# Kernel optimization log

Hardware: AMD Instinct MI355X
Metric: run time of the kernel (lower is better)

Reference implementation:

```python
import jax, jax.numpy as jnp
import numpy as np

N = 16384      # number of points
DIM = 128      # feature dim
POS_DIM = 3
K = 16         # neighbors (init kwarg k)
SCALE = np.float32(np.sqrt(DIM))


def setup_inputs() -> dict:
    key = jax.random.key(0)
    ks = jax.random.split(key, 16)
    g = lambda i, shape: (jax.random.normal(ks[i], shape, dtype=jnp.float32) * 0.05)
    return {
        "x": jax.random.normal(ks[0], (N, DIM), dtype=jnp.float32),
        "pos": jax.random.uniform(ks[1], (N, POS_DIM), dtype=jnp.float32),
        # weights stored as (in, out); torch Linear applies x @ W.T + b
        "Wq": g(2, (DIM, DIM)),
        "Wk": g(3, (DIM, DIM)),
        "Wv": g(4, (DIM, DIM)),
        "mid_w1": g(5, (DIM, DIM)), "mid_b1": g(6, (DIM,)),
        "mid_w2": g(7, (DIM, DIM)), "mid_b2": g(8, (DIM,)),
        "pe_w1": g(9, (POS_DIM, DIM)), "pe_b1": g(10, (DIM,)),
        "pe_w2": g(11, (DIM, DIM)), "pe_b2": g(12, (DIM,)),
        "fin_w": g(13, (DIM, DIM)), "fin_b": g(14, (DIM,)),
    }


def _knn_indices(pos):
    # squared pairwise distances [N, N]; top-K smallest -> neighbor indices [N, K]
    sq = jnp.sum(pos * pos, axis=-1)
    d2 = sq[:, None] + sq[None, :] - 2.0 * (pos @ pos.T)
    _, ind = jax.lax.top_k(-d2, K)
    return ind


def reference(x, pos, Wq, Wk, Wv, mid_w1, mid_b1, mid_w2, mid_b2,
              pe_w1, pe_b1, pe_w2, pe_b2, fin_w, fin_b):
    ind = _knn_indices(pos)                    # [N, K] int32 (constant wrt grads)
    x_k = x[ind]                               # [N, K, D]
    pos_k = pos[ind]                           # [N, K, 3]
    rel = pos[:, None, :] - pos_k              # [N, K, 3]
    pe = jax.nn.relu(rel @ pe_w1 + pe_b1) @ pe_w2 + pe_b2    # [N, K, D]
    q = x @ Wq                                 # [N, D]
    h = q[:, None, :] - (x_k @ Wk) + pe        # [N, K, D]
    y = jax.nn.relu(h @ mid_w1 + mid_b1) @ mid_w2 + mid_b2   # [N, K, D]
    y = jax.nn.softmax(y / SCALE, axis=-2)     # softmax over neighbors K
    z = x_k @ Wv + pe                          # [N, K, D]
    agg = jnp.sum(y * z, axis=-2)              # [N, D]
    return agg @ fin_w + fin_b + x
```

## Files before the change

kernel.cpp:

```cpp
#include <hip/hip_runtime.h>
#include <hip/hip_bf16.h>

#define N_PTS 16384
#define DIMF  128
#define KNB   16
#define GRES  8
#define NCELL (GRES*GRES*GRES)

typedef __attribute__((ext_vector_type(8))) short bf16x8;
typedef __attribute__((ext_vector_type(4))) short bf16x4;
typedef __attribute__((ext_vector_type(4))) float f32x4;
typedef __attribute__((ext_vector_type(4))) unsigned int u32x4;
typedef __attribute__((ext_vector_type(2))) unsigned int u32x2;

__device__ __forceinline__ unsigned short f2b(float f){
  unsigned int u = __float_as_uint(f);
  u = u + 0x7fffu + ((u >> 16) & 1u);
  return (unsigned short)(u >> 16);
}
__device__ __forceinline__ unsigned cvtpk(float lo, float hi){
  unsigned r;
  asm("v_cvt_pk_bf16_f32 %0, %1, %2" : "=v"(r) : "v"(lo), "v"(hi));
  return r;
}
__device__ __forceinline__ float b2f(unsigned short u){
  return __uint_as_float(((unsigned)u) << 16);
}
__device__ __forceinline__ float b2fs(short s){
  return __uint_as_float(((unsigned)(unsigned short)s) << 16);
}
__device__ __forceinline__ float unsort_f(unsigned s){
  unsigned u = (s & 0x80000000u) ? (s ^ 0x80000000u) : ~s;
  return __uint_as_float(u);
}

__global__ __launch_bounds__(256) void count_kernel(const float* __restrict__ pos, int* __restrict__ cnt){
  int i = blockIdx.x*256 + threadIdx.x;
  float px = pos[i*3+0], py = pos[i*3+1], pz = pos[i*3+2];
  int cx = min(GRES-1, max(0,(int)(px*(float)GRES)));
  int cy = min(GRES-1, max(0,(int)(py*(float)GRES)));
  int cz = min(GRES-1, max(0,(int)(pz*(float)GRES)));
  atomicAdd(&cnt[(cz*GRES+cy)*GRES+cx], 1);
}

__global__ __launch_bounds__(256) void scan_kernel(const int* __restrict__ cnt, int* __restrict__ starts, int* __restrict__ fillp){
  __shared__ int wsum[4];
  int t = threadIdx.x;
  int lane = t & 63, w = t >> 6;
  int a = cnt[2*t], b = cnt[2*t+1];
  int s = a + b;
  int p = s;
  #pragma unroll
  for (int off = 1; off < 64; off <<= 1){
    int v = __shfl_up(p, off, 64);
    if (lane >= off) p += v;
  }
  if (lane == 63) wsum[w] = p;
  __syncthreads();
  int base = 0;
  for (int i = 0; i < w; ++i) base += wsum[i];
  int excl = base + p - s;
  starts[2*t]   = excl;     fillp[2*t]   = excl;
  starts[2*t+1] = excl + a; fillp[2*t+1] = excl + a;
}

__global__ __launch_bounds__(256) void scatter_kernel(const float* __restrict__ pos, int* __restrict__ fillp,
                                                      float4* __restrict__ pos4, int* __restrict__ pidx,
                                                      int* __restrict__ inv){
  int i = blockIdx.x*256 + threadIdx.x;
  float px = pos[i*3+0], py = pos[i*3+1], pz = pos[i*3+2];
  int cx = min(GRES-1, max(0,(int)(px*(float)GRES)));
  int cy = min(GRES-1, max(0,(int)(py*(float)GRES)));
  int cz = min(GRES-1, max(0,(int)(pz*(float)GRES)));
  int c = (cz*GRES+cy)*GRES+cx;
  float sq = __fadd_rn(__fadd_rn(__fmul_rn(px,px), __fmul_rn(py,py)), __fmul_rn(pz,pz));
  int s = atomicAdd(&fillp[c], 1);
  pos4[s] = make_float4(px, py, pz, sq);
  pidx[s] = i;
  inv[i] = s;
}

__global__ __launch_bounds__(256) void knn_query64(const float4* __restrict__ pos4, const int* __restrict__ pidx,
                                                   const int* __restrict__ starts, const int* __restrict__ cnt,
                                                   const int* __restrict__ inv,
                                                   int* __restrict__ ind_slot, char* __restrict__ flags){
  __shared__ unsigned long long cand[4][64];
  int lane = threadIdx.x & 63;
  int wv   = threadIdx.x >> 6;
  int t = blockIdx.x*4 + wv;
  float4 qp = pos4[t];
  float qx = qp.x, qy = qp.y, qz = qp.z, qsq = qp.w;
  int cx = min(GRES-1, max(0,(int)(qx*(float)GRES)));
  int cy = min(GRES-1, max(0,(int)(qy*(float)GRES)));
  int cz = min(GRES-1, max(0,(int)(qz*(float)GRES)));
  int zlo = max(0,cz-1), zhi = min(GRES-1,cz+1);
  int ylo = max(0,cy-1), yhi = min(GRES-1,cy+1);
  int xlo = max(0,cx-1), xhi = min(GRES-1,cx+1);

  int nb = 0;
  if (lane < 27){
    int dz = lane/9 - 1, dy = (lane/3)%3 - 1, dx = lane%3 - 1;
    int zz = cz+dz, yy = cy+dy, xx = cx+dx;
    if (zz>=zlo && zz<=zhi && yy>=ylo && yy<=yhi && xx>=xlo && xx<=xhi)
      nb = cnt[(zz*GRES+yy)*GRES+xx];
  }
  #pragma unroll
  for (int o=1;o<64;o<<=1) nb += __shfl_xor(nb, o, 64);
  float V = (float)((zhi-zlo+1)*(yhi-ylo+1)*(xhi-xlo+1)) * 0.001953125f;
  float r3 = 3.8197186f * V / (float)nb;
  float tau2 = 2.0f * __powf(r3, 0.66666667f);

  int nfound = 0;
  bool okscan = false;
  for (int it = 0; it < 8; ++it){
    nfound = 0;
    for (int zz=zlo; zz<=zhi; ++zz)
    for (int yy=ylo; yy<=yhi; ++yy)
    for (int xx=xlo; xx<=xhi; ++xx){
      int c = (zz*GRES+yy)*GRES+xx;
      int s0 = starts[c], n = cnt[c];
      for (int b = 0; b < n; b += 64){
        int o = b + lane;
        bool valid = o < n;
        float d = 3.0e38f; int idx = 0;
        if (valid){
          float4 pc = pos4[s0+o];
          idx = pidx[s0+o];
          float dot = __fmaf_rn(qz, pc.z, __fmaf_rn(qy, pc.y, __fmul_rn(qx, pc.x)));
          d   = __fsub_rn(__fadd_rn(qsq, pc.w), __fmul_rn(2.0f, dot));
        }
        bool admit = valid && (d < tau2);
        unsigned long long mask = __ballot(admit);
        if (admit){
          int pos = nfound + (int)__popcll(mask & ((1ull<<lane)-1ull));
          if (pos < 64){
            unsigned su = __float_as_uint(d);
            su ^= (unsigned)((int)su >> 31) | 0x80000000u;
            cand[wv][pos] = ((unsigned long long)su << 32) | (unsigned)idx;
          }
        }
        nfound += (int)__popcll(mask);
      }
    }
    if (nfound > 64){ tau2 *= 0.7f; continue; }
    if (nfound < 16){ tau2 *= 2.0f; continue; }
    okscan = true; break;
  }
  if (!okscan){ if (lane == 0) flags[t] = 1; return; }

  asm volatile("s_waitcnt lgkmcnt(0)" ::: "memory");
  __builtin_amdgcn_sched_barrier(0);
  unsigned long long key = (lane < nfound) ? cand[wv][lane] : ~0ull;

  #pragma unroll
  for (int k = 2; k <= 64; k <<= 1){
    #pragma unroll
    for (int j = k>>1; j >= 1; j >>= 1){
      unsigned long long other = __shfl_xor(key, j, 64);
      bool takeSmall = (((lane & k) == 0) != ((lane & j) != 0));
      bool less = other < key;
      key = (takeSmall == less) ? other : key;
    }
  }
  if (lane < 16) ind_slot[t*KNB + lane] = inv[(int)(unsigned)(key & 0xffffffffu)];

  unsigned long long k15 = __shfl(key, 15, 64);
  float b16 = unsort_f((unsigned)(k15 >> 32));
  double mg = 1.0e300;
  double dqx=(double)qx, dqy=(double)qy, dqz=(double)qz;
  const double h = 0.125;
  if (cx-1 > 0)      mg = fmin(mg, dqx - (double)(cx-1)*h);
  if (cx+1 < GRES-1) mg = fmin(mg, (double)(cx+2)*h - dqx);
  if (cy-1 > 0)      mg = fmin(mg, dqy - (double)(cy-1)*h);
  if (cy+1 < GRES-1) mg = fmin(mg, (double)(cy+2)*h - dqy);
  if (cz-1 > 0)      mg = fmin(mg, dqz - (double)(cz-1)*h);
  if (cz+1 < GRES-1) mg = fmin(mg, (double)(cz+2)*h - dqz);
  bool ok = (mg*mg > (double)b16 + 1.0e-5);
  if (lane == 0) flags[t] = ok ? 0 : 1;
}

__global__ __launch_bounds__(256) void knn_fallback(const float4* __restrict__ pos4, const int* __restrict__ pidx,
                                                    const int* __restrict__ starts, const int* __restrict__ cnt,
                                                    const int* __restrict__ inv,
                                                    const char* __restrict__ flags, int* __restrict__ ind_slot){
  int t = blockIdx.x*256 + threadIdx.x;
  if (t >= N_PTS || !flags[t]) return;
  float4 qp = pos4[t];
  float qx = qp.x, qy = qp.y, qz = qp.z, qsq = qp.w;
  int cx = min(GRES-1, max(0,(int)(qx*(float)GRES)));
  int cy = min(GRES-1, max(0,(int)(qy*(float)GRES)));
  int cz = min(GRES-1, max(0,(int)(qz*(float)GRES)));
  float bd[KNB]; int bi[KNB];
  #pragma unroll
  for (int k=0;k<KNB;++k){ bd[k] = 3.0e38f; bi[k] = 0x7fffffff; }
  const double cinv = 0.125;
  for (int r = 0; r < GRES; ++r){
    int zlo = max(0, cz-r), zhi = min(GRES-1, cz+r);
    int ylo = max(0, cy-r), yhi = min(GRES-1, cy+r);
    int xlo = max(0, cx-r), xhi = min(GRES-1, cx+r);
    for (int zz = zlo; zz <= zhi; ++zz){
      for (int yy = ylo; yy <= yhi; ++yy){
        for (int xx = xlo; xx <= xhi; ++xx){
          int ring = max(abs(zz-cz), max(abs(yy-cy), abs(xx-cx)));
          if (ring != r) continue;
          int c = (zz*GRES+yy)*GRES+xx;
          int s0 = starts[c], e = s0 + cnt[c];
          for (int s = s0; s < e; ++s){
            float4 pc = pos4[s];
            int idx = pidx[s];
            float dot = __fmaf_rn(qz, pc.z, __fmaf_rn(qy, pc.y, __fmul_rn(qx, pc.x)));
            float d   = __fsub_rn(__fadd_rn(qsq, pc.w), __fmul_rn(2.0f, dot));
            bool adm = (d < bd[KNB-1]) || (d == bd[KNB-1] && idx < bi[KNB-1]);
            if (adm){
              #pragma unroll
              for (int p = KNB-1; p >= 1; --p){
                float pd = bd[p-1]; int pi = bi[p-1];
                bool sh  = (pd > d) || (pd == d && pi > idx);
                bool ins = (!sh) && ((bd[p] > d) || (bd[p] == d && bi[p] > idx));
                bd[p] = sh ? pd : (ins ? d   : bd[p]);
                bi[p] = sh ? pi : (ins ? idx : bi[p]);
              }
              bool s0b = (bd[0] > d) || (bd[0] == d && bi[0] > idx);
              if (s0b){ bd[0] = d; bi[0] = idx; }
            }
          }
        }
      }
    }
    if (bd[KNB-1] < 3.0e37f){
      double mg = 1.0e300;
      double dqx=(double)qx, dqy=(double)qy, dqz=(double)qz;
      if (cx - r > 0)      mg = fmin(mg, dqx - (double)(cx-r)*cinv);
      if (cx + r < GRES-1) mg = fmin(mg, (double)(cx+r+1)*cinv - dqx);
      if (cy - r > 0)      mg = fmin(mg, dqy - (double)(cy-r)*cinv);
      if (cy + r < GRES-1) mg = fmin(mg, (double)(cy+r+1)*cinv - dqy);
      if (cz - r > 0)      mg = fmin(mg, dqz - (double)(cz-r)*cinv);
      if (cz + r < GRES-1) mg = fmin(mg, (double)(cz+r+1)*cinv - dqz);
      if (mg*mg > (double)bd[KNB-1] + 1.0e-5) break;
    }
  }
  #pragma unroll
  for (int k=0;k<KNB;++k) ind_slot[t*KNB + k] = inv[bi[k]];
}

__global__ __launch_bounds__(256) void pack_all(const float* __restrict__ w0, const float* __restrict__ w1,
                                                const float* __restrict__ w2, const float* __restrict__ w3,
                                                const float* __restrict__ w4, const float* __restrict__ w5,
                                                const float* __restrict__ w6,
                                                short* __restrict__ dst){
  int slot = blockIdx.y;
  const float* src = (slot==0)?w0:(slot==1)?w1:(slot==2)?w2:(slot==3)?w3:(slot==4)?w4:(slot==5)?w5:w6;
  int f = blockIdx.x*256 + threadIdx.x;
  int j  = f & 7;
  int ln = (f >> 3) & 63;
  int ks = (f >> 9) & 3;
  int nt = f >> 11;
  int k = ks*32 + ((ln >> 4) << 3) + j;
  int n = nt*16 + (ln & 15);
  dst[slot*16384 + f] = (short)f2b(src[k*DIMF + n]);
}

__global__ __launch_bounds__(256) void proj_kernel(const float* __restrict__ x, const int* __restrict__ pidx,
                                                   const short* __restrict__ pw,
                                                   unsigned short* __restrict__ q, unsigned short* __restrict__ xk,
                                                   unsigned short* __restrict__ xv){
  __shared__ __align__(16) char Abuf[16384];
  int tid = threadIdx.x, lane = tid & 63, wv = tid >> 6;
  int r0 = blockIdx.x * 64;
  {
    int row = tid >> 2, q4 = tid & 3;
    int orig = pidx[r0 + row];
    const float4* xr = (const float4*)(x + (size_t)orig*DIMF + q4*32);
    #pragma unroll
    for (int i=0;i<4;++i){
      float4 a = xr[2*i], b = xr[2*i+1];
      u32x4 u;
      u[0] = cvtpk(a.x, a.y); u[1] = cvtpk(a.z, a.w);
      u[2] = cvtpk(b.x, b.y); u[3] = cvtpk(b.z, b.w);
      *(u32x4*)(&Abuf[row*256 + ((q4*64 + i*16) ^ ((row&7)<<4))]) = u;
    }
  }
  __syncthreads();
  #pragma unroll 1
  for (int w = 0; w < 3; ++w){
    const bf16x8* bw = (const bf16x8*)(pw + w*16384);
    unsigned short* dst = (w==0) ? q : (w==1) ? xk : xv;
    f32x4 acc[8];
    #pragma unroll
    for (int nt=0;nt<8;++nt) acc[nt] = (f32x4){0.f,0.f,0.f,0.f};
    #pragma unroll
    for (int ks=0;ks<4;++ks){
      int ra = wv*16 + (lane&15);
      int cb = ks*64 + ((lane>>4)<<4);
      bf16x8 a0 = *(const bf16x8*)(&Abuf[ra*256 + (cb ^ ((ra&7)<<4))]);
      #pragma unroll
      for (int nt=0;nt<8;++nt){
        bf16x8 b = bw[(nt*4+ks)*64 + lane];
        acc[nt] = __builtin_amdgcn_mfma_f32_16x16x32_bf16(a0, b, acc[nt], 0, 0, 0);
      }
    }
    #pragma unroll
    for (int nt=0;nt<8;++nt){
      int grow = r0 + wv*16 + ((lane>>4)<<2);
      int col = nt*16 + (lane&15);
      unsigned pk01 = cvtpk(acc[nt][0], acc[nt][1]);
      unsigned pk23 = cvtpk(acc[nt][2], acc[nt][3]);
      dst[(size_t)(grow+0)*DIMF + col] = (unsigned short)pk01;
      dst[(size_t)(grow+1)*DIMF + col] = (unsigned short)(pk01 >> 16);
      dst[(size_t)(grow+2)*DIMF + col] = (unsigned short)pk23;
      dst[(size_t)(grow+3)*DIMF + col] = (unsigned short)(pk23 >> 16);
    }
  }
}

__global__ __launch_bounds__(512, 2) void main_kernel(
    const float* __restrict__ x, const float4* __restrict__ pos4, const int* __restrict__ pidx,
    const float* __restrict__ pe_w1, const float* __restrict__ pe_b1, const float* __restrict__ pe_b2,
    const float* __restrict__ mid_b1, const float* __restrict__ mid_b2, const float* __restrict__ fin_b,
    const unsigned short* __restrict__ qarr, const unsigned short* __restrict__ xkarr,
    const unsigned short* __restrict__ xvarr,
    const int* __restrict__ ind_slot, const short* __restrict__ pw,
    float* __restrict__ out)
{
  __shared__ __align__(16) char peLDS[32768];
  __shared__ __align__(16) char wbuf[32768];
  __shared__ float aggT[DIMF][9];
  __shared__ int indbuf[128];
  __shared__ int origbuf[8];
  int tid = threadIdx.x;
  int lane = tid & 63;
  int wv = tid >> 6;
  int t0 = blockIdx.x * 8;

  int g = lane >> 4, kl = lane & 15;
  int mt = wv;

  #define STAGE_W(slot) { \
    const char* gsrc = (const char*)(pw + (size_t)(slot)*16384) + wv*4096 + lane*16; \
    char* ldst = &wbuf[wv*4096]; \
    __builtin_amdgcn_global_load_lds(gsrc,        ldst,        16, 0, 0); \
    __builtin_amdgcn_global_load_lds(gsrc + 1024, ldst + 1024, 16, 0, 0); \
    __builtin_amdgcn_global_load_lds(gsrc + 2048, ldst + 2048, 16, 0, 0); \
    __builtin_amdgcn_global_load_lds(gsrc + 3072, ldst + 3072, 16, 0, 0); }

  if (tid < 128) indbuf[tid] = ind_slot[blockIdx.x*128 + tid];
  if (tid < 8) origbuf[tid] = pidx[t0 + tid];
  STAGE_W(3);
  __syncthreads();

  int nb4[4];
  #pragma unroll
  for (int r=0;r<4;++r) nb4[r] = indbuf[mt*16 + g*4 + r];
  int nbr = indbuf[mt*16 + kl];
  unsigned short zraw[8][4];
  #pragma unroll
  for (int nt=0;nt<8;++nt)
    #pragma unroll
    for (int r=0;r<4;++r)
      zraw[nt][r] = xvarr[(size_t)nb4[r]*DIMF + nt*16 + kl];

  bf16x8 tfrag[4];
  {
    float4 pq = pos4[t0+mt];
    float4 pn = pos4[nbr];
    float rx = pq.x-pn.x, ry = pq.y-pn.y, rz = pq.z-pn.z;
    #pragma unroll
    for (int ks=0;ks<4;++ks){
      int c0 = ks*32 + g*8;
      const float4* w0 = (const float4*)(pe_w1 + c0);
      const float4* w1 = (const float4*)(pe_w1 + DIMF + c0);
      const float4* w2 = (const float4*)(pe_w1 + 2*DIMF + c0);
      const float4* bb = (const float4*)(pe_b1 + c0);
      float4 wa0=w0[0], wa1=w0[1], wb0=w1[0], wb1=w1[1], wc0=w2[0], wc1=w2[1], wd0=bb[0], wd1=bb[1];
      float wa[8]={wa0.x,wa0.y,wa0.z,wa0.w,wa1.x,wa1.y,wa1.z,wa1.w};
      float wb[8]={wb0.x,wb0.y,wb0.z,wb0.w,wb1.x,wb1.y,wb1.z,wb1.w};
      float wc[8]={wc0.x,wc0.y,wc0.z,wc0.w,wc1.x,wc1.y,wc1.z,wc1.w};
      float wd[8]={wd0.x,wd0.y,wd0.z,wd0.w,wd1.x,wd1.y,wd1.z,wd1.w};
      float tv[8];
      #pragma unroll
      for (int j=0;j<8;++j)
        tv[j] = fmaxf(fmaf(rx, wa[j], fmaf(ry, wb[j], fmaf(rz, wc[j], wd[j]))), 0.f);
      u32x4 u;
      u[0] = cvtpk(tv[0], tv[1]); u[1] = cvtpk(tv[2], tv[3]);
      u[2] = cvtpk(tv[4], tv[5]); u[3] = cvtpk(tv[6], tv[7]);
      tfrag[ks] = __builtin_bit_cast(bf16x8, u);
    }
  }

  f32x4 acc[8];
  const bf16x8* bw = (const bf16x8*)wbuf;

  {
    #pragma unroll
    for (int nt=0;nt<8;++nt){
      float bv = pe_b2[nt*16 + kl];
      acc[nt] = (f32x4){bv,bv,bv,bv};
    }
    #pragma unroll
    for (int ks=0;ks<4;++ks){
      #pragma unroll
      for (int nt=0;nt<8;++nt){
        bf16x8 b = bw[(nt*4+ks)*64 + lane];
        acc[nt] = __builtin_amdgcn_mfma_f32_16x16x32_bf16(tfrag[ks], b, acc[nt], 0, 0, 0);
      }
    }
  }

  bf16x4 zb[8];
  int r0w = mt*16 + g*4;
  #pragma unroll
  for (int nt=0;nt<8;++nt){
    int col = nt*16 + kl;
    float p0 = acc[nt][0], p1 = acc[nt][1], p2 = acc[nt][2], p3 = acc[nt][3];
    unsigned pk01 = cvtpk(p0, p1), pk23 = cvtpk(p2, p3);
    *(unsigned short*)&peLDS[(r0w+0)*256 + ((col*2) ^ (((r0w+0)&7)<<4))] = (unsigned short)pk01;
    *(unsigned short*)&peLDS[(r0w+1)*256 + ((col*2) ^ (((r0w+1)&7)<<4))] = (unsigned short)(pk01 >> 16);
    *(unsigned short*)&peLDS[(r0w+2)*256 + ((col*2) ^ (((r0w+2)&7)<<4))] = (unsigned short)pk23;
    *(unsigned short*)&peLDS[(r0w+3)*256 + ((col*2) ^ (((r0w+3)&7)<<4))] = (unsigned short)(pk23 >> 16);
    float z0 = b2f(zraw[nt][0]) + p0;
    float z1 = b2f(zraw[nt][1]) + p1;
    float z2 = b2f(zraw[nt][2]) + p2;
    float z3 = b2f(zraw[nt][3]) + p3;
    u32x2 zu; zu[0] = cvtpk(z0, z1); zu[1] = cvtpk(z2, z3);
    zb[nt] = __builtin_bit_cast(bf16x4, zu);
  }

  bf16x8 q8[4], k8[4];
  {
    const unsigned short* qrow = qarr + (size_t)(t0+mt)*DIMF;
    const unsigned short* krow = xkarr + (size_t)nbr*DIMF;
    #pragma unroll
    for (int ks=0;ks<4;++ks){
      int c0 = ks*32 + g*8;
      q8[ks] = *(const bf16x8*)(qrow + c0);
      k8[ks] = *(const bf16x8*)(krow + c0);
    }
  }
  __syncthreads();
  STAGE_W(4);

  bf16x8 hfrag[4];
  {
    int row = mt*16 + kl;
    #pragma unroll
    for (int ks=0;ks<4;++ks){
      int c0 = ks*32 + g*8;
      bf16x8 p8 = *(const bf16x8*)(&peLDS[row*256 + ((c0*2) ^ ((row&7)<<4))]);
      float hf[8];
      #pragma unroll
      for (int j=0;j<8;++j)
        hf[j] = (b2fs(q8[ks][j]) - b2fs(k8[ks][j])) + b2fs(p8[j]);
      u32x4 u;
      u[0] = cvtpk(hf[0], hf[1]); u[1] = cvtpk(hf[2], hf[3]);
      u[2] = cvtpk(hf[4], hf[5]); u[3] = cvtpk(hf[6], hf[7]);
      hfrag[ks] = __builtin_bit_cast(bf16x8, u);
    }
  }
  __syncthreads();

  {
    #pragma unroll
    for (int nt=0;nt<8;++nt){
      float bv = mid_b1[nt*16 + kl];
      acc[nt] = (f32x4){bv,bv,bv,bv};
    }
    #pragma unroll
    for (int ks=0;ks<4;++ks){
      #pragma unroll
      for (int nt=0;nt<8;++nt){
        bf16x8 b = bw[(nt*4+ks)*64 + lane];
        acc[nt] = __builtin_amdgcn_mfma_f32_16x16x32_bf16(hfrag[ks], b, acc[nt], 0, 0, 0);
      }
    }
  }
  __syncthreads();
  STAGE_W(5);
  #pragma unroll
  for (int nt=0;nt<8;++nt){
    int col = nt*16 + kl;
    unsigned pk01 = cvtpk(fmaxf(acc[nt][0],0.f), fmaxf(acc[nt][1],0.f));
    unsigned pk23 = cvtpk(fmaxf(acc[nt][2],0.f), fmaxf(acc[nt][3],0.f));
    *(unsigned short*)&peLDS[(r0w+0)*256 + ((col*2) ^ (((r0w+0)&7)<<4))] = (unsigned short)pk01;
    *(unsigned short*)&peLDS[(r0w+1)*256 + ((col*2) ^ (((r0w+1)&7)<<4))] = (unsigned short)(pk01 >> 16);
    *(unsigned short*)&peLDS[(r0w+2)*256 + ((col*2) ^ (((r0w+2)&7)<<4))] = (unsigned short)pk23;
    *(unsigned short*)&peLDS[(r0w+3)*256 + ((col*2) ^ (((r0w+3)&7)<<4))] = (unsigned short)(pk23 >> 16);
  }
  __syncthreads();

  {
    #pragma unroll
    for (int nt=0;nt<8;++nt){
      float bv = mid_b2[nt*16 + kl];
      acc[nt] = (f32x4){bv,bv,bv,bv};
    }
    #pragma unroll
    for (int ks=0;ks<4;++ks){
      int ra = mt*16 + kl;
      int cb = ks*64 + g*16;
      bf16x8 a0 = *(const bf16x8*)(&peLDS[ra*256 + (cb ^ ((ra&7)<<4))]);
      #pragma unroll
      for (int nt=0;nt<8;++nt){
        bf16x8 b = bw[(nt*4+ks)*64 + lane];
        acc[nt] = __builtin_amdgcn_mfma_f32_16x16x32_bf16(a0, b, acc[nt], 0, 0, 0);
      }
    }
  }
  __syncthreads();
  STAGE_W(6);

  {
    const float invS = 0.08838834764831843f;
    #pragma unroll
    for (int nt=0;nt<8;++nt){
      f32x4 y = acc[nt];
      float mx = fmaxf(fmaxf(y[0],y[1]), fmaxf(y[2],y[3]));
      mx = fmaxf(mx, __shfl_xor(mx, 16, 64));
      mx = fmaxf(mx, __shfl_xor(mx, 32, 64));
      float e0 = __expf((y[0]-mx)*invS);
      float e1 = __expf((y[1]-mx)*invS);
      float e2 = __expf((y[2]-mx)*invS);
      float e3 = __expf((y[3]-mx)*invS);
      float ssum = e0+e1+e2+e3;
      ssum += __shfl_xor(ssum, 16, 64);
      ssum += __shfl_xor(ssum, 32, 64);
      bf16x4 zv = zb[nt];
      float ps = (e0*b2fs(zv[0]) + e1*b2fs(zv[1]) + e2*b2fs(zv[2]) + e3*b2fs(zv[3])) / ssum;
      ps += __shfl_xor(ps, 16, 64);
      ps += __shfl_xor(ps, 32, 64);
      if (lane < 16) aggT[nt*16 + lane][mt] = ps;
    }
  }
  __syncthreads();

  {
    f32x4 facc = (f32x4){0.f,0.f,0.f,0.f};
    #pragma unroll
    for (int ks=0;ks<4;++ks){
      int c0 = ks*32 + g*8;
      float av[8];
      #pragma unroll
      for (int j=0;j<8;++j)
        av[j] = (kl < 8) ? aggT[c0+j][kl] : 0.f;
      u32x4 u;
      u[0] = cvtpk(av[0], av[1]); u[1] = cvtpk(av[2], av[3]);
      u[2] = cvtpk(av[4], av[5]); u[3] = cvtpk(av[6], av[7]);
      bf16x8 a = __builtin_bit_cast(bf16x8, u);
      bf16x8 b = bw[(wv*4+ks)*64 + lane];
      facc = __builtin_amdgcn_mfma_f32_16x16x32_bf16(a, b, facc, 0, 0, 0);
    }
    int col = wv*16 + kl;
    float fb = fin_b[col];
    if (g < 2){
      #pragma unroll
      for (int r=0;r<4;++r){
        int prow = g*4 + r;
        int o = origbuf[prow];
        out[(size_t)o*DIMF + col] = facc[r] + fb + x[(size_t)o*DIMF + col];
      }
    }
  }
  #undef STAGE_W
}

extern "C" void kernel_launch(void* const* d_in, const int* in_sizes, int n_in,
                              void* d_out, int out_size, void* d_ws, size_t ws_size,
                              hipStream_t stream)
{
  (void)in_sizes; (void)n_in; (void)out_size; (void)ws_size;
  const float* x      = (const float*)d_in[0];
  const float* pos    = (const float*)d_in[1];
  const float* Wq     = (const float*)d_in[2];
  const float* Wk     = (const float*)d_in[3];
  const float* Wv     = (const float*)d_in[4];
  const float* mid_w1 = (const float*)d_in[5];
  const float* mid_b1 = (const float*)d_in[6];
  const float* mid_w2 = (const float*)d_in[7];
  const float* mid_b2 = (const float*)d_in[8];
  const float* pe_w1  = (const float*)d_in[9];
  const float* pe_b1  = (const float*)d_in[10];
  const float* pe_w2  = (const float*)d_in[11];
  const float* pe_b2  = (const float*)d_in[12];
  const float* fin_w  = (const float*)d_in[13];
  const float* fin_b  = (const float*)d_in[14];
  float* out = (float*)d_out;
  char* ws = (char*)d_ws;

  int*    cellcnt = (int*)   (ws + 0);
  int*    fillp   = (int*)   (ws + 4096);
  int*    starts  = (int*)   (ws + 8192);
  char*   flags   = (char*)  (ws + 18432);
  int*    pidx    = (int*)   (ws + 49152);
  float4* pos4    = (float4*)(ws + 114688);
  int*    ind     = (int*)   (ws + 376832);
  short*  pw      = (short*) (ws + 1425408);
  int*    inv     = (int*)   (ws + 1654784);
  unsigned short* qarr  = (unsigned short*)(ws + 1720320);
  unsigned short* xkarr = (unsigned short*)(ws + 5914624);
  unsigned short* xvarr = (unsigned short*)(ws + 10108928);

  hipMemsetAsync(cellcnt, 0, NCELL*sizeof(int), stream);
  count_kernel  <<<N_PTS/256, 256, 0, stream>>>(pos, cellcnt);
  scan_kernel   <<<1,         256, 0, stream>>>(cellcnt, starts, fillp);
  scatter_kernel<<<N_PTS/256, 256, 0, stream>>>(pos, fillp, pos4, pidx, inv);
  knn_query64   <<<N_PTS/4,   256, 0, stream>>>(pos4, pidx, starts, cellcnt, inv, ind, flags);
  knn_fallback  <<<N_PTS/256, 256, 0, stream>>>(pos4, pidx, starts, cellcnt, inv, flags, ind);

  pack_all<<<dim3(64,7), 256, 0, stream>>>(Wq, Wk, Wv, pe_w2, mid_w1, mid_w2, fin_w, pw);

  proj_kernel<<<N_PTS/64, 256, 0, stream>>>(x, pidx, pw, qarr, xkarr, xvarr);

  main_kernel<<<N_PTS/8, 512, 0, stream>>>(x, pos4, pidx, pe_w1, pe_b1, pe_b2, mid_b1, mid_b2, fin_b,
                                           qarr, xkarr, xvarr, ind, pw, out);
}
```

Before: 164.9 us.

## Merge grid build with weight packing and kNN query with projection kernels

Replaces the memset, count and scan kernels with one block that counts points into cells in LDS and scans them. The remaining blocks of that launch pack the weights. The kNN query and the Q/K/V projection now run as disjoint block ranges of a single launch. This cuts the launch count from 8 to 5 and lets independent work overlap. The trade-off is that a single block now counts all 16384 points serially, and the fused kernel carries the larger LDS footprint for every block.

```diff
diff --git a/kernel.cpp b/kernel.cpp
--- a/kernel.cpp
+++ b/kernel.cpp
@@ -34,34 +34,57 @@
   return __uint_as_float(u);
 }
 
-__global__ __launch_bounds__(256) void count_kernel(const float* __restrict__ pos, int* __restrict__ cnt){
-  int i = blockIdx.x*256 + threadIdx.x;
-  float px = pos[i*3+0], py = pos[i*3+1], pz = pos[i*3+2];
-  int cx = min(GRES-1, max(0,(int)(px*(float)GRES)));
-  int cy = min(GRES-1, max(0,(int)(py*(float)GRES)));
-  int cz = min(GRES-1, max(0,(int)(pz*(float)GRES)));
-  atomicAdd(&cnt[(cz*GRES+cy)*GRES+cx], 1);
-}
-
-__global__ __launch_bounds__(256) void scan_kernel(const int* __restrict__ cnt, int* __restrict__ starts, int* __restrict__ fillp){
+__global__ __launch_bounds__(256) void build_pack(const float* __restrict__ pos,
+                                                  int* __restrict__ cnt, int* __restrict__ starts, int* __restrict__ fillp,
+                                                  const float* __restrict__ w0, const float* __restrict__ w1,
+                                                  const float* __restrict__ w2, const float* __restrict__ w3,
+                                                  const float* __restrict__ w4, const float* __restrict__ w5,
+                                                  const float* __restrict__ w6,
+                                                  short* __restrict__ dst){
+  __shared__ int lcnt[NCELL];
   __shared__ int wsum[4];
-  int t = threadIdx.x;
-  int lane = t & 63, w = t >> 6;
-  int a = cnt[2*t], b = cnt[2*t+1];
-  int s = a + b;
-  int p = s;
-  #pragma unroll
-  for (int off = 1; off < 64; off <<= 1){
-    int v = __shfl_up(p, off, 64);
-    if (lane >= off) p += v;
-  }
-  if (lane == 63) wsum[w] = p;
-  __syncthreads();
-  int base = 0;
-  for (int i = 0; i < w; ++i) base += wsum[i];
-  int excl = base + p - s;
-  starts[2*t]   = excl;     fillp[2*t]   = excl;
-  starts[2*t+1] = excl + a; fillp[2*t+1] = excl + a;
+  if (blockIdx.x == 0){
+    int t = threadIdx.x;
+    lcnt[2*t] = 0; lcnt[2*t+1] = 0;
+    __syncthreads();
+    for (int i = t; i < N_PTS; i += 256){
+      float px = pos[i*3+0], py = pos[i*3+1], pz = pos[i*3+2];
+      int cx = min(GRES-1, max(0,(int)(px*(float)GRES)));
+      int cy = min(GRES-1, max(0,(int)(py*(float)GRES)));
+      int cz = min(GRES-1, max(0,(int)(pz*(float)GRES)));
+      atomicAdd(&lcnt[(cz*GRES+cy)*GRES+cx], 1);
+    }
+    __syncthreads();
+    int lane = t & 63, w = t >> 6;
+    int a = lcnt[2*t], b = lcnt[2*t+1];
+    int s = a + b;
+    int p = s;
+    #pragma unroll
+    for (int off = 1; off < 64; off <<= 1){
+      int v = __shfl_up(p, off, 64);
+      if (lane >= off) p += v;
+    }
+    if (lane == 63) wsum[w] = p;
+    __syncthreads();
+    int base = 0;
+    for (int i = 0; i < w; ++i) base += wsum[i];
+    int excl = base + p - s;
+    cnt[2*t] = a;           cnt[2*t+1] = b;
+    starts[2*t]   = excl;   fillp[2*t]   = excl;
+    starts[2*t+1] = excl+a; fillp[2*t+1] = excl+a;
+  } else {
+    int pb = blockIdx.x - 1;
+    int slot = pb >> 6;
+    const float* src = (slot==0)?w0:(slot==1)?w1:(slot==2)?w2:(slot==3)?w3:(slot==4)?w4:(slot==5)?w5:w6;
+    int f = (pb & 63)*256 + threadIdx.x;
+    int j  = f & 7;
+    int ln = (f >> 3) & 63;
+    int ks = (f >> 9) & 3;
+    int nt = f >> 11;
+    int k = ks*32 + ((ln >> 4) << 3) + j;
+    int n = nt*16 + (ln & 15);
+    dst[slot*16384 + f] = (short)f2b(src[k*DIMF + n]);
+  }
 }
 
 __global__ __launch_bounds__(256) void scatter_kernel(const float* __restrict__ pos, int* __restrict__ fillp,
@@ -80,103 +103,156 @@
   inv[i] = s;
 }
 
-__global__ __launch_bounds__(256) void knn_query64(const float4* __restrict__ pos4, const int* __restrict__ pidx,
-                                                   const int* __restrict__ starts, const int* __restrict__ cnt,
-                                                   const int* __restrict__ inv,
-                                                   int* __restrict__ ind_slot, char* __restrict__ flags){
+__global__ __launch_bounds__(256) void knn_proj(const float4* __restrict__ pos4, const int* __restrict__ pidx,
+                                                const int* __restrict__ starts, const int* __restrict__ cnt,
+                                                const int* __restrict__ inv,
+                                                int* __restrict__ ind_slot, char* __restrict__ flags,
+                                                const float* __restrict__ x, const short* __restrict__ pw,
+                                                unsigned short* __restrict__ q, unsigned short* __restrict__ xk,
+                                                unsigned short* __restrict__ xv){
   __shared__ unsigned long long cand[4][64];
-  int lane = threadIdx.x & 63;
-  int wv   = threadIdx.x >> 6;
-  int t = blockIdx.x*4 + wv;
-  float4 qp = pos4[t];
-  float qx = qp.x, qy = qp.y, qz = qp.z, qsq = qp.w;
-  int cx = min(GRES-1, max(0,(int)(qx*(float)GRES)));
-  int cy = min(GRES-1, max(0,(int)(qy*(float)GRES)));
-  int cz = min(GRES-1, max(0,(int)(qz*(float)GRES)));
-  int zlo = max(0,cz-1), zhi = min(GRES-1,cz+1);
-  int ylo = max(0,cy-1), yhi = min(GRES-1,cy+1);
-  int xlo = max(0,cx-1), xhi = min(GRES-1,cx+1);
-
-  int nb = 0;
-  if (lane < 27){
-    int dz = lane/9 - 1, dy = (lane/3)%3 - 1, dx = lane%3 - 1;
-    int zz = cz+dz, yy = cy+dy, xx = cx+dx;
-    if (zz>=zlo && zz<=zhi && yy>=ylo && yy<=yhi && xx>=xlo && xx<=xhi)
-      nb = cnt[(zz*GRES+yy)*GRES+xx];
-  }
-  #pragma unroll
-  for (int o=1;o<64;o<<=1) nb += __shfl_xor(nb, o, 64);
-  float V = (float)((zhi-zlo+1)*(yhi-ylo+1)*(xhi-xlo+1)) * 0.001953125f;
-  float r3 = 3.8197186f * V / (float)nb;
-  float tau2 = 2.0f * __powf(r3, 0.66666667f);
-
-  int nfound = 0;
-  bool okscan = false;
-  for (int it = 0; it < 8; ++it){
-    nfound = 0;
-    for (int zz=zlo; zz<=zhi; ++zz)
-    for (int yy=ylo; yy<=yhi; ++yy)
-    for (int xx=xlo; xx<=xhi; ++xx){
-      int c = (zz*GRES+yy)*GRES+xx;
-      int s0 = starts[c], n = cnt[c];
-      for (int b = 0; b < n; b += 64){
-        int o = b + lane;
-        bool valid = o < n;
-        float d = 3.0e38f; int idx = 0;
-        if (valid){
-          float4 pc = pos4[s0+o];
-          idx = pidx[s0+o];
-          float dot = __fmaf_rn(qz, pc.z, __fmaf_rn(qy, pc.y, __fmul_rn(qx, pc.x)));
-          d   = __fsub_rn(__fadd_rn(qsq, pc.w), __fmul_rn(2.0f, dot));
+  __shared__ __align__(16) char Abuf[16384];
+  if (blockIdx.x < N_PTS/4){
+    int lane = threadIdx.x & 63;
+    int wv   = threadIdx.x >> 6;
+    int t = blockIdx.x*4 + wv;
+    float4 qp = pos4[t];
+    float qx = qp.x, qy = qp.y, qz = qp.z, qsq = qp.w;
+    int cx = min(GRES-1, max(0,(int)(qx*(float)GRES)));
+    int cy = min(GRES-1, max(0,(int)(qy*(float)GRES)));
+    int cz = min(GRES-1, max(0,(int)(qz*(float)GRES)));
+    int zlo = max(0,cz-1), zhi = min(GRES-1,cz+1);
+    int ylo = max(0,cy-1), yhi = min(GRES-1,cy+1);
+    int xlo = max(0,cx-1), xhi = min(GRES-1,cx+1);
+
+    int nb = 0;
+    if (lane < 27){
+      int dz = lane/9 - 1, dy = (lane/3)%3 - 1, dx = lane%3 - 1;
+      int zz = cz+dz, yy = cy+dy, xx = cx+dx;
+      if (zz>=zlo && zz<=zhi && yy>=ylo && yy<=yhi && xx>=xlo && xx<=xhi)
+        nb = cnt[(zz*GRES+yy)*GRES+xx];
+    }
+    #pragma unroll
+    for (int o=1;o<64;o<<=1) nb += __shfl_xor(nb, o, 64);
+    float V = (float)((zhi-zlo+1)*(yhi-ylo+1)*(xhi-xlo+1)) * 0.001953125f;
+    float r3 = 3.8197186f * V / (float)nb;
+    float tau2 = 2.0f * __powf(r3, 0.66666667f);
+
+    int nfound = 0;
+    bool okscan = false;
+    for (int it = 0; it < 8; ++it){
+      nfound = 0;
+      for (int zz=zlo; zz<=zhi; ++zz)
+      for (int yy=ylo; yy<=yhi; ++yy)
+      for (int xx=xlo; xx<=xhi; ++xx){
+        int c = (zz*GRES+yy)*GRES+xx;
+        int s0 = starts[c], n = cnt[c];
+        for (int b = 0; b < n; b += 64){
+          int o = b + lane;
+          bool valid = o < n;
+          float d = 3.0e38f; int idx = 0;
+          if (valid){
+            float4 pc = pos4[s0+o];
+            idx = pidx[s0+o];
+            float dot = __fmaf_rn(qz, pc.z, __fmaf_rn(qy, pc.y, __fmul_rn(qx, pc.x)));
+            d   = __fsub_rn(__fadd_rn(qsq, pc.w), __fmul_rn(2.0f, dot));
+          }
+          bool admit = valid && (d < tau2);
+          unsigned long long mask = __ballot(admit);
+          if (admit){
+            int pos = nfound + (int)__popcll(mask & ((1ull<<lane)-1ull));
+            if (pos < 64){
+              unsigned su = __float_as_uint(d);
+              su ^= (unsigned)((int)su >> 31) | 0x80000000u;
+              cand[wv][pos] = ((unsigned long long)su << 32) | (unsigned)idx;
+            }
+          }
+          nfound += (int)__popcll(mask);
         }
-        bool admit = valid && (d < tau2);
-        unsigned long long mask = __ballot(admit);
-        if (admit){
-          int pos = nfound + (int)__popcll(mask & ((1ull<<lane)-1ull));
-          if (pos < 64){
-            unsigned su = __float_as_uint(d);
-            su ^= (unsigned)((int)su >> 31) | 0x80000000u;
-            cand[wv][pos] = ((unsigned long long)su << 32) | (unsigned)idx;
-          }
+      }
+      if (nfound > 64){ tau2 *= 0.7f; continue; }
+      if (nfound < 16){ tau2 *= 2.0f; continue; }
+      okscan = true; break;
+    }
+    if (!okscan){ if (lane == 0) flags[t] = 1; return; }
+
+    asm volatile("s_waitcnt lgkmcnt(0)" ::: "memory");
+    __builtin_amdgcn_sched_barrier(0);
+    unsigned long long key = (lane < nfound) ? cand[wv][lane] : ~0ull;
+
+    #pragma unroll
+    for (int k = 2; k <= 64; k <<= 1){
+      #pragma unroll
+      for (int j = k>>1; j >= 1; j >>= 1){
+        unsigned long long other = __shfl_xor(key, j, 64);
+        bool takeSmall = (((lane & k) == 0) != ((lane & j) != 0));
+        bool less = other < key;
+        key = (takeSmall == less) ? other : key;
+      }
+    }
+    if (lane < 16) ind_slot[t*KNB + lane] = inv[(int)(unsigned)(key & 0xffffffffu)];
+
+    unsigned long long k15 = __shfl(key, 15, 64);
+    float b16 = unsort_f((unsigned)(k15 >> 32));
+    double mg = 1.0e300;
+    double dqx=(double)qx, dqy=(double)qy, dqz=(double)qz;
+    const double h = 0.125;
+    if (cx-1 > 0)      mg = fmin(mg, dqx - (double)(cx-1)*h);
+    if (cx+1 < GRES-1) mg = fmin(mg, (double)(cx+2)*h - dqx);
+    if (cy-1 > 0)      mg = fmin(mg, dqy - (double)(cy-1)*h);
+    if (cy+1 < GRES-1) mg = fmin(mg, (double)(cy+2)*h - dqy);
+    if (cz-1 > 0)      mg = fmin(mg, dqz - (double)(cz-1)*h);
+    if (cz+1 < GRES-1) mg = fmin(mg, (double)(cz+2)*h - dqz);
+    bool ok = (mg*mg > (double)b16 + 1.0e-5);
+    if (lane == 0) flags[t] = ok ? 0 : 1;
+  } else {
+    int tid = threadIdx.x, lane = tid & 63, wv = tid >> 6;
+    int r0 = (blockIdx.x - N_PTS/4) * 64;
+    {
+      int row = tid >> 2, q4 = tid & 3;
+      int orig = pidx[r0 + row];
+      const float4* xr = (const float4*)(x + (size_t)orig*DIMF + q4*32);
+      #pragma unroll
+      for (int i=0;i<4;++i){
+        float4 a = xr[2*i], b = xr[2*i+1];
+        u32x4 u;
+        u[0] = cvtpk(a.x, a.y); u[1] = cvtpk(a.z, a.w);
+        u[2] = cvtpk(b.x, b.y); u[3] = cvtpk(b.z, b.w);
+        *(u32x4*)(&Abuf[row*256 + ((q4*64 + i*16) ^ ((row&7)<<4))]) = u;
+      }
+    }
+    __syncthreads();
+    #pragma unroll 1
+    for (int w = 0; w < 3; ++w){
+      const bf16x8* bw = (const bf16x8*)(pw + w*16384);
+      unsigned short* dst = (w==0) ? q : (w==1) ? xk : xv;
+      f32x4 acc[8];
+      #pragma unroll
+      for (int nt=0;nt<8;++nt) acc[nt] = (f32x4){0.f,0.f,0.f,0.f};
+      #pragma unroll
+      for (int ks=0;ks<4;++ks){
+        int ra = wv*16 + (lane&15);
+        int cb = ks*64 + ((lane>>4)<<4);
+        bf16x8 a0 = *(const bf16x8*)(&Abuf[ra*256 + (cb ^ ((ra&7)<<4))]);
+        #pragma unroll
+        for (int nt=0;nt<8;++nt){
+          bf16x8 b = bw[(nt*4+ks)*64 + lane];
+          acc[nt] = __builtin_amdgcn_mfma_f32_16x16x32_bf16(a0, b, acc[nt], 0, 0, 0);
         }
-        nfound += (int)__popcll(mask);
-      }
-    }
-    if (nfound > 64){ tau2 *= 0.7f; continue; }
-    if (nfound < 16){ tau2 *= 2.0f; continue; }
-    okscan = true; break;
-  }
-  if (!okscan){ if (lane == 0) flags[t] = 1; return; }
-
-  asm volatile("s_waitcnt lgkmcnt(0)" ::: "memory");
-  __builtin_amdgcn_sched_barrier(0);
-  unsigned long long key = (lane < nfound) ? cand[wv][lane] : ~0ull;
-
-  #pragma unroll
-  for (int k = 2; k <= 64; k <<= 1){
-    #pragma unroll
-    for (int j = k>>1; j >= 1; j >>= 1){
-      unsigned long long other = __shfl_xor(key, j, 64);
-      bool takeSmall = (((lane & k) == 0) != ((lane & j) != 0));
-      bool less = other < key;
-      key = (takeSmall == less) ? other : key;
-    }
-  }
-  if (lane < 16) ind_slot[t*KNB + lane] = inv[(int)(unsigned)(key & 0xffffffffu)];
-
-  unsigned long long k15 = __shfl(key, 15, 64);
-  float b16 = unsort_f((unsigned)(k15 >> 32));
-  double mg = 1.0e300;
-  double dqx=(double)qx, dqy=(double)qy, dqz=(double)qz;
-  const double h = 0.125;
-  if (cx-1 > 0)      mg = fmin(mg, dqx - (double)(cx-1)*h);
-  if (cx+1 < GRES-1) mg = fmin(mg, (double)(cx+2)*h - dqx);
-  if (cy-1 > 0)      mg = fmin(mg, dqy - (double)(cy-1)*h);
-  if (cy+1 < GRES-1) mg = fmin(mg, (double)(cy+2)*h - dqy);
-  if (cz-1 > 0)      mg = fmin(mg, dqz - (double)(cz-1)*h);
-  if (cz+1 < GRES-1) mg = fmin(mg, (double)(cz+2)*h - dqz);
-  bool ok = (mg*mg > (double)b16 + 1.0e-5);
-  if (lane == 0) flags[t] = ok ? 0 : 1;
+      }
+      #pragma unroll
+      for (int nt=0;nt<8;++nt){
+        int grow = r0 + wv*16 + ((lane>>4)<<2);
+        int col = nt*16 + (lane&15);
+        unsigned pk01 = cvtpk(acc[nt][0], acc[nt][1]);
+        unsigned pk23 = cvtpk(acc[nt][2], acc[nt][3]);
+        dst[(size_t)(grow+0)*DIMF + col] = (unsigned short)pk01;
+        dst[(size_t)(grow+1)*DIMF + col] = (unsigned short)(pk01 >> 16);
+        dst[(size_t)(grow+2)*DIMF + col] = (unsigned short)pk23;
+        dst[(size_t)(grow+3)*DIMF + col] = (unsigned short)(pk23 >> 16);
+      }
+    }
+  }
 }
 
 __global__ __launch_bounds__(256) void knn_fallback(const float4* __restrict__ pos4, const int* __restrict__ pidx,
@@ -243,76 +319,6 @@
   for (int k=0;k<KNB;++k) ind_slot[t*KNB + k] = inv[bi[k]];
 }
 
-__global__ __launch_bounds__(256) void pack_all(const float* __restrict__ w0, const float* __restrict__ w1,
-                                                const float* __restrict__ w2, const float* __restrict__ w3,
-                                                const float* __restrict__ w4, const float* __restrict__ w5,
-                                                const float* __restrict__ w6,
-                                                short* __restrict__ dst){
-  int slot = blockIdx.y;
-  const float* src = (slot==0)?w0:(slot==1)?w1:(slot==2)?w2:(slot==3)?w3:(slot==4)?w4:(slot==5)?w5:w6;
-  int f = blockIdx.x*256 + threadIdx.x;
-  int j  = f & 7;
-  int ln = (f >> 3) & 63;
-  int ks = (f >> 9) & 3;
-  int nt = f >> 11;
-  int k = ks*32 + ((ln >> 4) << 3) + j;
-  int n = nt*16 + (ln & 15);
-  dst[slot*16384 + f] = (short)f2b(src[k*DIMF + n]);
-}
-
-__global__ __launch_bounds__(256) void proj_kernel(const float* __restrict__ x, const int* __restrict__ pidx,
-                                                   const short* __restrict__ pw,
-                                                   unsigned short* __restrict__ q, unsigned short* __restrict__ xk,
-                                                   unsigned short* __restrict__ xv){
-  __shared__ __align__(16) char Abuf[16384];
-  int tid = threadIdx.x, lane = tid & 63, wv = tid >> 6;
-  int r0 = blockIdx.x * 64;
-  {
-    int row = tid >> 2, q4 = tid & 3;
-    int orig = pidx[r0 + row];
-    const float4* xr = (const float4*)(x + (size_t)orig*DIMF + q4*32);
-    #pragma unroll
-    for (int i=0;i<4;++i){
-      float4 a = xr[2*i], b = xr[2*i+1];
-      u32x4 u;
-      u[0] = cvtpk(a.x, a.y); u[1] = cvtpk(a.z, a.w);
-      u[2] = cvtpk(b.x, b.y); u[3] = cvtpk(b.z, b.w);
-      *(u32x4*)(&Abuf[row*256 + ((q4*64 + i*16) ^ ((row&7)<<4))]) = u;
-    }
-  }
-  __syncthreads();
-  #pragma unroll 1
-  for (int w = 0; w < 3; ++w){
-    const bf16x8* bw = (const bf16x8*)(pw + w*16384);
-    unsigned short* dst = (w==0) ? q : (w==1) ? xk : xv;
-    f32x4 acc[8];
-    #pragma unroll
-    for (int nt=0;nt<8;++nt) acc[nt] = (f32x4){0.f,0.f,0.f,0.f};
-    #pragma unroll
-    for (int ks=0;ks<4;++ks){
-      int ra = wv*16 + (lane&15);
-      int cb = ks*64 + ((lane>>4)<<4);
-      bf16x8 a0 = *(const bf16x8*)(&Abuf[ra*256 + (cb ^ ((ra&7)<<4))]);
-      #pragma unroll
-      for (int nt=0;nt<8;++nt){
-        bf16x8 b = bw[(nt*4+ks)*64 + lane];
-        acc[nt] = __builtin_amdgcn_mfma_f32_16x16x32_bf16(a0, b, acc[nt], 0, 0, 0);
-      }
-    }
-    #pragma unroll
-    for (int nt=0;nt<8;++nt){
-      int grow = r0 + wv*16 + ((lane>>4)<<2);
-      int col = nt*16 + (lane&15);
-      unsigned pk01 = cvtpk(acc[nt][0], acc[nt][1]);
-      unsigned pk23 = cvtpk(acc[nt][2], acc[nt][3]);
-      dst[(size_t)(grow+0)*DIMF + col] = (unsigned short)pk01;
-      dst[(size_t)(grow+1)*DIMF + col] = (unsigned short)(pk01 >> 16);
-      dst[(size_t)(grow+2)*DIMF + col] = (unsigned short)pk23;
-      dst[(size_t)(grow+3)*DIMF + col] = (unsigned short)(pk23 >> 16);
-    }
-  }
-}
-
 __global__ __launch_bounds__(512, 2) void main_kernel(
     const float* __restrict__ x, const float4* __restrict__ pos4, const int* __restrict__ pidx,
     const float* __restrict__ pe_w1, const float* __restrict__ pe_b1, const float* __restrict__ pe_b2,
@@ -598,17 +604,12 @@
   unsigned short* xkarr = (unsigned short*)(ws + 5914624);
   unsigned short* xvarr = (unsigned short*)(ws + 10108928);
 
-  hipMemsetAsync(cellcnt, 0, NCELL*sizeof(int), stream);
-  count_kernel  <<<N_PTS/256, 256, 0, stream>>>(pos, cellcnt);
-  scan_kernel   <<<1,         256, 0, stream>>>(cellcnt, starts, fillp);
+  build_pack    <<<1 + 7*64,  256, 0, stream>>>(pos, cellcnt, starts, fillp,
+                                                Wq, Wk, Wv, pe_w2, mid_w1, mid_w2, fin_w, pw);
   scatter_kernel<<<N_PTS/256, 256, 0, stream>>>(pos, fillp, pos4, pidx, inv);
-  knn_query64   <<<N_PTS/4,   256, 0, stream>>>(pos4, pidx, starts, cellcnt, inv, ind, flags);
+  knn_proj      <<<N_PTS/4 + N_PTS/64, 256, 0, stream>>>(pos4, pidx, starts, cellcnt, inv, ind, flags,
+                                                         x, pw, qarr, xkarr, xvarr);
   knn_fallback  <<<N_PTS/256, 256, 0, stream>>>(pos4, pidx, starts, cellcnt, inv, flags, ind);
-
-  pack_all<<<dim3(64,7), 256, 0, stream>>>(Wq, Wk, Wv, pe_w2, mid_w1, mid_w2, fin_w, pw);
-
-  proj_kernel<<<N_PTS/64, 256, 0, stream>>>(x, pidx, pw, qarr, xkarr, xvarr);
-
-  main_kernel<<<N_PTS/8, 512, 0, stream>>>(x, pos4, pidx, pe_w1, pe_b1, pe_b2, mid_b1, mid_b2, fin_b,
-                                           qarr, xkarr, xvarr, ind, pw, out);
-}
+  main_kernel   <<<N_PTS/8,   512, 0, stream>>>(x, pos4, pidx, pe_w1, pe_b1, pe_b2, mid_b1, mid_b2, fin_b,
+                                                qarr, xkarr, xvarr, ind, pw, out);
+}
```

After: 178.7 us. 8.4% more time.
